# Kernel optimization log

Hardware: AMD Instinct MI355X
Metric: run time of the kernel (lower is better)

The kernel has to match this reference:

```python
import jax, jax.numpy as jnp
from jax import lax
import numpy as np


def setup_inputs() -> dict:
    key = jax.random.key(0)
    k1, k2, k3, k4, k5 = jax.random.split(key, 5)
    bs, m, v, L, P = 2, 16, 16, 40320, 32
    preds = jax.random.normal(k1, (bs, m, v, L), dtype=jnp.float32)
    target = jax.random.normal(k2, (bs, v, L), dtype=jnp.float32)
    weights = jax.random.uniform(k3, (L,), dtype=jnp.float32)
    scale = jax.random.uniform(k4, (v,), dtype=jnp.float32)
    # binary-ish patch masks over grid points (float, as in the torch buffer)
    masks = (jax.random.uniform(k5, (P, L)) < 0.25).astype(jnp.float32)
    return {"preds": preds, "target": target, "weights": weights,
            "scale": scale, "masks": masks, "beta": 1}


def _energy_score(x, y, m, beta):
    # x: (bs, m, D) ensemble, y: (bs, D) observation
    diff = x - y[:, None, :]
    a = jnp.sqrt(jnp.sum(diff * diff, axis=-1))            # (bs, m)
    score_a = jnp.mean(jnp.sum(a ** beta, axis=-1)) / m
    # pairwise distances via Gram trick (cdist p=2)
    sq = jnp.sum(x * x, axis=-1)                            # (bs, m)
    g = jnp.einsum('bid,bjd->bij', x, x)                    # (bs, m, m)
    d2 = jnp.maximum(sq[:, :, None] + sq[:, None, :] - 2.0 * g, 0.0)
    pos = d2 > 0
    d = jnp.where(pos, jnp.sqrt(jnp.where(pos, d2, 1.0)), 0.0)
    score_b = jnp.mean(jnp.sum(d ** beta, axis=(1, 2))) / (2 * m * (m - 1))
    return score_a - score_b


def reference(preds, target, weights, scale, masks, beta):
    beta = float(beta)
    bs, m, v, L = preds.shape
    # buffer scaling as in forward()
    p = preds * scale[None, None, :, None] * weights        # (bs, m, v, L)
    t = target * scale[None, :, None] * weights             # (bs, v, L)

    def body(acc, mask):
        # rearrange 'bs m v latlon -> bs m (latlon v)'
        x = (p * mask).transpose(0, 1, 3, 2).reshape(bs, m, L * v)
        y = (t * mask).transpose(0, 2, 1).reshape(bs, L * v)
        return acc + _energy_score(x, y, m, beta), None

    total, _ = lax.scan(body, jnp.float32(0.0), masks)
    return total
```

## Files before the change

### kernel.cpp

```cpp
#include <hip/hip_runtime.h>
#include <math.h>

#define BS 2
#define M 16
#define V 16
#define NROWB 136
#define NROWS 272
#define PMASK 32
#define KZ 32
#define KSTEPS 1260
#define NWORK 128

typedef __attribute__((ext_vector_type(8))) short bf16x8;
typedef __attribute__((ext_vector_type(4))) float f32x4;

static __device__ __forceinline__ unsigned short f2bf(float x) {
    unsigned int u = __float_as_uint(x);
    unsigned int r = (u + 0x7FFFu + ((u >> 16) & 1u)) >> 16;
    return (unsigned short)r;
}

template<int W>
static __device__ __forceinline__ void k1_compute(
    const float (*__restrict__ xs)[64],
    const float* __restrict__ target,
    const float* __restrict__ scale, float wl,
    int b, int lane, int l0, int L,
    unsigned short* __restrict__ S)
{
    float acc[34];
#pragma unroll
    for (int r = 0; r < 34; ++r) acc[r] = 0.0f;

    const int base = (W == 0) ? 0 : 34 * W - 16;
    const int npair = (W == 0) ? 18 : 34;
    const int aoff = (W == 0) ? 16 : 0;

    for (int v = 0; v < V; ++v) {
        float sw = scale[v] * wl;
        float x[M];
#pragma unroll
        for (int i = 0; i < M; ++i)
            x[i] = xs[i * 16 + v][lane] * sw;
        if (W == 0) {
            float y = target[(size_t)(b * V + v) * L + l0 + lane] * sw;
#pragma unroll
            for (int i = 0; i < M; ++i) {
                float d = x[i] - y;
                acc[i] = fmaf(d, d, acc[i]);
            }
        }
        int k = 0;
#pragma unroll
        for (int i = 0; i < M; ++i) {
#pragma unroll
            for (int j = i + 1; j < M; ++j) {
                if (k >= base && k < base + npair) {
                    float d = x[i] - x[j];
                    acc[aoff + k - base] = fmaf(d, d, acc[aoff + k - base]);
                }
                ++k;
            }
        }
    }
#pragma unroll
    for (int r = 0; r < 34; ++r)
        S[(size_t)(b * NROWB + 34 * W + r) * L + l0 + lane] = f2bf(acc[r]);
}

__global__ __launch_bounds__(256, 2)
void k1_pairsums(const float* __restrict__ preds, const float* __restrict__ target,
                 const float* __restrict__ weights, const float* __restrict__ scale,
                 const float* __restrict__ masks,
                 unsigned short* __restrict__ S, unsigned short* __restrict__ maskbf,
                 int L)
{
    __shared__ float xs[256][64];
    int t = (int)threadIdx.x;
    int lane = t & 63, wave = t >> 6;
    int l0 = (int)blockIdx.x * 64;
    int b = (int)blockIdx.y;

    const float* pbase = preds + (size_t)b * 256 * L + l0;
#pragma unroll
    for (int n = 0; n < 16; ++n) {
        int r0 = wave * 64 + n * 4;
        const float* g = pbase + (size_t)(r0 + (lane >> 4)) * L + (lane & 15) * 4;
        __builtin_amdgcn_global_load_lds(
            (const __attribute__((address_space(1))) unsigned int*)g,
            (__attribute__((address_space(3))) unsigned int*)&xs[r0][0],
            16, 0, 0);
    }

    if (b == 0) {
#pragma unroll
        for (int pp = 0; pp < 8; ++pp) {
            int p = wave * 8 + pp;
            maskbf[(size_t)p * L + l0 + lane] =
                (masks[(size_t)p * L + l0 + lane] != 0.0f) ? (unsigned short)0x3F80
                                                           : (unsigned short)0;
        }
    }

    float wl = weights[l0 + lane];
    __syncthreads();

    switch (wave) {
        case 0: k1_compute<0>(xs, target, scale, wl, b, lane, l0, L, S); break;
        case 1: k1_compute<1>(xs, target, scale, wl, b, lane, l0, L, S); break;
        case 2: k1_compute<2>(xs, target, scale, wl, b, lane, l0, L, S); break;
        default: k1_compute<3>(xs, target, scale, wl, b, lane, l0, L, S); break;
    }
}

__global__ __launch_bounds__(256, 4)
void k2_mfma(const unsigned short* __restrict__ S,
             const unsigned short* __restrict__ maskbf,
             float* __restrict__ D2p, int L)
{
    int lane = (int)(threadIdx.x & 63);
    int wave = (int)(threadIdx.x >> 6);
    int mtile = blockIdx.x;
    int z = blockIdx.y;
    int zw = z * 4 + wave;

    const int q = KSTEPS / NWORK;
    const int rem = KSTEPS % NWORK;
    int start = zw * q + (zw < rem ? zw : rem);
    int cnt = q + (zw < rem ? 1 : 0);

    const unsigned short* Arow =
        S + (size_t)(mtile * 16 + (lane & 15)) * L + (lane >> 4) * 8;
    const unsigned short* B0 =
        maskbf + (size_t)(lane & 15) * L + (lane >> 4) * 8;
    const unsigned short* B1 =
        maskbf + (size_t)(16 + (lane & 15)) * L + (lane >> 4) * 8;

    f32x4 acc0 = {0.f, 0.f, 0.f, 0.f};
    f32x4 acc1 = {0.f, 0.f, 0.f, 0.f};

    for (int s = 0; s < cnt; ++s) {
        int k0 = (start + s) * 32;
        bf16x8 a  = *(const bf16x8*)(Arow + k0);
        bf16x8 b0 = *(const bf16x8*)(B0 + k0);
        bf16x8 b1 = *(const bf16x8*)(B1 + k0);
        acc0 = __builtin_amdgcn_mfma_f32_16x16x32_bf16(a, b0, acc0, 0, 0, 0);
        acc1 = __builtin_amdgcn_mfma_f32_16x16x32_bf16(a, b1, acc1, 0, 0, 0);
    }

    __shared__ float red[4][512];
    int c16 = lane & 15;
#pragma unroll
    for (int reg = 0; reg < 4; ++reg) {
        int r16 = (lane >> 4) * 4 + reg;
        red[wave][r16 * 16 + c16]       = acc0[reg];
        red[wave][256 + r16 * 16 + c16] = acc1[reg];
    }
    __syncthreads();
    int t = (int)threadIdx.x;
#pragma unroll
    for (int u = t; u < 512; u += 256) {
        float v = red[0][u] + red[1][u] + red[2][u] + red[3][u];
        D2p[((size_t)z * 17 + mtile) * 512 + u] = v;
    }
}

__global__ __launch_bounds__(256, 2)
void k3_finalize(const float* __restrict__ D2p, const int* __restrict__ beta_p,
                 float* __restrict__ out)
{
    int t = (int)threadIdx.x;
    int e = blockIdx.x * 256 + t;
    int mtile = e >> 9;
    int flat = e & 511;

    float vbuf[KZ];
#pragma unroll
    for (int z = 0; z < KZ; ++z)
        vbuf[z] = D2p[((size_t)z * 17 + mtile) * 512 + flat];

    float a0 = 0.f, a1 = 0.f, a2 = 0.f, a3 = 0.f;
#pragma unroll
    for (int z = 0; z < KZ; z += 4) {
        a0 += vbuf[z + 0]; a1 += vbuf[z + 1];
        a2 += vbuf[z + 2]; a3 += vbuf[z + 3];
    }
    float d2 = fmaxf((a0 + a1) + (a2 + a3), 0.0f);
    float beta = (float)beta_p[0];
    float d = (beta == 1.0f) ? sqrtf(d2) : powf(d2, 0.5f * beta);

    const float wa = 1.0f / (float)(BS * M);
    const float wb = -1.0f / (float)(BS * M * (M - 1));
    int row = mtile * 16 + ((flat >> 4) & 15);
    int local = row % NROWB;
    float sum = ((local < M) ? wa : wb) * d;

    int lane = t & 63, wv = t >> 6;
#pragma unroll
    for (int off = 32; off > 0; off >>= 1)
        sum += __shfl_down(sum, off, 64);
    __shared__ float red[4];
    if (lane == 0) red[wv] = sum;
    __syncthreads();
    if (t == 0)
        atomicAdd(out, red[0] + red[1] + red[2] + red[3]);
}

extern "C" void kernel_launch(void* const* d_in, const int* in_sizes, int n_in,
                              void* d_out, int out_size, void* d_ws, size_t ws_size,
                              hipStream_t stream)
{
    const float* preds   = (const float*)d_in[0];
    const float* target  = (const float*)d_in[1];
    const float* weights = (const float*)d_in[2];
    const float* scale   = (const float*)d_in[3];
    const float* masks   = (const float*)d_in[4];
    const int*   beta    = (const int*)d_in[5];
    float* out = (float*)d_out;

    int L = in_sizes[2];

    unsigned short* S = (unsigned short*)d_ws;
    size_t s_bytes = (size_t)NROWS * (size_t)L * sizeof(unsigned short);
    unsigned short* maskbf = (unsigned short*)((char*)d_ws + ((s_bytes + 255) & ~(size_t)255));
    size_t m_bytes = (size_t)PMASK * (size_t)L * sizeof(unsigned short);
    float* D2p = (float*)((char*)maskbf + ((m_bytes + 255) & ~(size_t)255));

    hipMemsetAsync(out, 0, sizeof(float), stream);

    dim3 g1(L / 64, BS);
    k1_pairsums<<<g1, 256, 0, stream>>>(preds, target, weights, scale, masks,
                                        S, maskbf, L);

    dim3 g2(17, KZ);
    k2_mfma<<<g2, 256, 0, stream>>>(S, maskbf, D2p, L);

    k3_finalize<<<(NROWS * PMASK) / 256, 256, 0, stream>>>(D2p, beta, out);
}
```

Baseline: 160.8 us.

## Double-buffer preds tiles in k1 and split pair work across eight half-waves

```diff
diff --git a/kernel.cpp b/kernel.cpp
--- a/kernel.cpp
+++ b/kernel.cpp
@@ -10,6 +10,7 @@
 #define KZ 32
 #define KSTEPS 1260
 #define NWORK 128
+#define TPB 5
 
 typedef __attribute__((ext_vector_type(8))) short bf16x8;
 typedef __attribute__((ext_vector_type(4))) float f32x4;
@@ -20,30 +21,48 @@
     return (unsigned short)r;
 }
 
-template<int W>
+
+static __device__ __forceinline__ void k1_stage(
+    const float* __restrict__ preds, float* __restrict__ dst,
+    int b, int l0t, int L, int lane, int wave)
+{
+#pragma unroll
+    for (int n = 0; n < 8; ++n) {
+        int chunk = wave * 8 + n;
+        int r0 = chunk * 8;
+        const float* g = preds + (size_t)(b * 256 + r0 + (lane >> 3)) * L
+                         + l0t + (lane & 7) * 4;
+        __builtin_amdgcn_global_load_lds(
+            (const __attribute__((address_space(1))) unsigned int*)g,
+            (__attribute__((address_space(3))) unsigned int*)(dst + chunk * 256),
+            16, 0, 0);
+    }
+}
+
+template<int G>
 static __device__ __forceinline__ void k1_compute(
-    const float (*__restrict__ xs)[64],
-    const float* __restrict__ target,
+    const float* __restrict__ xsb,
+    const float* __restrict__ tg,
     const float* __restrict__ scale, float wl,
-    int b, int lane, int l0, int L,
+    int b, int li, int l, int L,
     unsigned short* __restrict__ S)
 {
-    float acc[34];
-#pragma unroll
-    for (int r = 0; r < 34; ++r) acc[r] = 0.0f;
-
-    const int base = (W == 0) ? 0 : 34 * W - 16;
-    const int npair = (W == 0) ? 18 : 34;
-    const int aoff = (W == 0) ? 16 : 0;
+    float acc[17];
+#pragma unroll
+    for (int r = 0; r < 17; ++r) acc[r] = 0.0f;
+
+    const int base = (G == 0) ? 0 : 17 * G - 16;
+    const int npair = (G == 0) ? 1 : 17;
+    const int aoff = (G == 0) ? 16 : 0;
 
     for (int v = 0; v < V; ++v) {
         float sw = scale[v] * wl;
         float x[M];
 #pragma unroll
         for (int i = 0; i < M; ++i)
-            x[i] = xs[i * 16 + v][lane] * sw;
-        if (W == 0) {
-            float y = target[(size_t)(b * V + v) * L + l0 + lane] * sw;
+            x[i] = xsb[(i * 16 + v) * 32 + li] * sw;
+        if (G == 0) {
+            float y = tg[v] * sw;
 #pragma unroll
             for (int i = 0; i < M; ++i) {
                 float d = x[i] - y;
@@ -64,8 +83,8 @@
         }
     }
 #pragma unroll
-    for (int r = 0; r < 34; ++r)
-        S[(size_t)(b * NROWB + 34 * W + r) * L + l0 + lane] = f2bf(acc[r]);
+    for (int r = 0; r < 17; ++r)
+        S[(size_t)(b * NROWB + 17 * G + r) * L + l] = f2bf(acc[r]);
 }
 
 __global__ __launch_bounds__(256, 2)
@@ -75,49 +94,70 @@
                  unsigned short* __restrict__ S, unsigned short* __restrict__ maskbf,
                  int L)
 {
-    __shared__ float xs[256][64];
+    __shared__ float xs[2][8192];
     int t = (int)threadIdx.x;
     int lane = t & 63, wave = t >> 6;
-    int l0 = (int)blockIdx.x * 64;
+    int g = t >> 5, li = t & 31;
+    int tile0 = (int)blockIdx.x * TPB;
     int b = (int)blockIdx.y;
 
-    const float* pbase = preds + (size_t)b * 256 * L + l0;
-#pragma unroll
-    for (int n = 0; n < 16; ++n) {
-        int r0 = wave * 64 + n * 4;
-        const float* g = pbase + (size_t)(r0 + (lane >> 4)) * L + (lane & 15) * 4;
-        __builtin_amdgcn_global_load_lds(
-            (const __attribute__((address_space(1))) unsigned int*)g,
-            (__attribute__((address_space(3))) unsigned int*)&xs[r0][0],
-            16, 0, 0);
-    }
-
-    if (b == 0) {
-#pragma unroll
-        for (int pp = 0; pp < 8; ++pp) {
-            int p = wave * 8 + pp;
-            maskbf[(size_t)p * L + l0 + lane] =
-                (masks[(size_t)p * L + l0 + lane] != 0.0f) ? (unsigned short)0x3F80
-                                                           : (unsigned short)0;
-        }
-    }
-
-    float wl = weights[l0 + lane];
-    __syncthreads();
-
-    switch (wave) {
-        case 0: k1_compute<0>(xs, target, scale, wl, b, lane, l0, L, S); break;
-        case 1: k1_compute<1>(xs, target, scale, wl, b, lane, l0, L, S); break;
-        case 2: k1_compute<2>(xs, target, scale, wl, b, lane, l0, L, S); break;
-        default: k1_compute<3>(xs, target, scale, wl, b, lane, l0, L, S); break;
+    k1_stage(preds, &xs[0][0], b, tile0 * 32, L, lane, wave);
+
+    for (int it = 0; it < TPB; ++it) {
+        int l0t = (tile0 + it) * 32;
+        int l = l0t + li;
+
+        float wl = weights[l];
+        float tg[V];
+        if (g == 0) {
+#pragma unroll
+            for (int v = 0; v < V; ++v)
+                tg[v] = target[(size_t)(b * V + v) * L + l];
+        }
+        unsigned short mk[4];
+        if (b == 0) {
+#pragma unroll
+            for (int pp = 0; pp < 4; ++pp) {
+                int p = g * 4 + pp;
+                mk[pp] = (masks[(size_t)p * L + l] != 0.0f) ? (unsigned short)0x3F80
+                                                            : (unsigned short)0;
+            }
+        }
+
+        __syncthreads();
+
+        if (it + 1 < TPB)
+            k1_stage(preds, &xs[(it + 1) & 1][0], b, (tile0 + it + 1) * 32, L,
+                     lane, wave);
+
+        if (b == 0) {
+#pragma unroll
+            for (int pp = 0; pp < 4; ++pp)
+                maskbf[(size_t)(g * 4 + pp) * L + l] = mk[pp];
+        }
+
+        const float* xsb = &xs[it & 1][0];
+        switch (g) {
+            case 0: k1_compute<0>(xsb, tg, scale, wl, b, li, l, L, S); break;
+            case 1: k1_compute<1>(xsb, tg, scale, wl, b, li, l, L, S); break;
+            case 2: k1_compute<2>(xsb, tg, scale, wl, b, li, l, L, S); break;
+            case 3: k1_compute<3>(xsb, tg, scale, wl, b, li, l, L, S); break;
+            case 4: k1_compute<4>(xsb, tg, scale, wl, b, li, l, L, S); break;
+            case 5: k1_compute<5>(xsb, tg, scale, wl, b, li, l, L, S); break;
+            case 6: k1_compute<6>(xsb, tg, scale, wl, b, li, l, L, S); break;
+            default: k1_compute<7>(xsb, tg, scale, wl, b, li, l, L, S); break;
+        }
     }
 }
 
 __global__ __launch_bounds__(256, 4)
 void k2_mfma(const unsigned short* __restrict__ S,
              const unsigned short* __restrict__ maskbf,
-             float* __restrict__ D2p, int L)
-{
+             float* __restrict__ D2p, float* __restrict__ out, int L)
+{
+    if (blockIdx.x == 0 && blockIdx.y == 0 && threadIdx.x == 0)
+        out[0] = 0.0f;
+
     int lane = (int)(threadIdx.x & 63);
     int wave = (int)(threadIdx.x >> 6);
     int mtile = blockIdx.x;
@@ -226,14 +266,12 @@
     size_t m_bytes = (size_t)PMASK * (size_t)L * sizeof(unsigned short);
     float* D2p = (float*)((char*)maskbf + ((m_bytes + 255) & ~(size_t)255));
 
-    hipMemsetAsync(out, 0, sizeof(float), stream);
-
-    dim3 g1(L / 64, BS);
+    dim3 g1((L / 32) / TPB, BS);
     k1_pairsums<<<g1, 256, 0, stream>>>(preds, target, weights, scale, masks,
                                         S, maskbf, L);
 
     dim3 g2(17, KZ);
-    k2_mfma<<<g2, 256, 0, stream>>>(S, maskbf, D2p, L);
+    k2_mfma<<<g2, 256, 0, stream>>>(S, maskbf, D2p, out, L);
 
     k3_finalize<<<(NROWS * PMASK) / 256, 256, 0, stream>>>(D2p, beta, out);
 }
```

New measurement: 225.7 us. +40.4%, slower.

## Stage preds in two half-variable chunks to halve LDS and raise occupancy

Applied to the files above, without the earlier changes.

```diff
diff --git a/kernel.cpp b/kernel.cpp
--- a/kernel.cpp
+++ b/kernel.cpp
@@ -20,28 +20,44 @@
     return (unsigned short)r;
 }
 
+
+static __device__ __forceinline__ void k1_stage(
+    const float* __restrict__ preds, float* __restrict__ dst,
+    int b, int v0, int l0, int L, int lane, int wave)
+{
+#pragma unroll
+    for (int n = 0; n < 8; ++n) {
+        int r0 = wave * 32 + n * 4;
+        int grow = b * 256 + (r0 >> 3) * 16 + v0 + (r0 & 7);
+        const float* g = preds + (size_t)(grow + (lane >> 4)) * L
+                         + l0 + (lane & 15) * 4;
+        __builtin_amdgcn_global_load_lds(
+            (const __attribute__((address_space(1))) unsigned int*)g,
+            (__attribute__((address_space(3))) unsigned int*)(dst + r0 * 64),
+            16, 0, 0);
+    }
+}
+
 template<int W>
-static __device__ __forceinline__ void k1_compute(
+static __device__ __forceinline__ void k1_chunk(
     const float (*__restrict__ xs)[64],
     const float* __restrict__ target,
     const float* __restrict__ scale, float wl,
-    int b, int lane, int l0, int L,
-    unsigned short* __restrict__ S)
-{
-    float acc[34];
-#pragma unroll
-    for (int r = 0; r < 34; ++r) acc[r] = 0.0f;
-
+    int b, int lane, int l0, int L, int v0,
+    float* __restrict__ acc)
+{
     const int base = (W == 0) ? 0 : 34 * W - 16;
     const int npair = (W == 0) ? 18 : 34;
     const int aoff = (W == 0) ? 16 : 0;
 
-    for (int v = 0; v < V; ++v) {
+#pragma unroll
+    for (int vc = 0; vc < 8; ++vc) {
+        int v = v0 + vc;
         float sw = scale[v] * wl;
         float x[M];
 #pragma unroll
         for (int i = 0; i < M; ++i)
-            x[i] = xs[i * 16 + v][lane] * sw;
+            x[i] = xs[i * 8 + vc][lane] * sw;
         if (W == 0) {
             float y = target[(size_t)(b * V + v) * L + l0 + lane] * sw;
 #pragma unroll
@@ -63,35 +79,24 @@
             }
         }
     }
-#pragma unroll
-    for (int r = 0; r < 34; ++r)
-        S[(size_t)(b * NROWB + 34 * W + r) * L + l0 + lane] = f2bf(acc[r]);
-}
-
-__global__ __launch_bounds__(256, 2)
+}
+
+__global__ __launch_bounds__(256, 4)
 void k1_pairsums(const float* __restrict__ preds, const float* __restrict__ target,
                  const float* __restrict__ weights, const float* __restrict__ scale,
                  const float* __restrict__ masks,
                  unsigned short* __restrict__ S, unsigned short* __restrict__ maskbf,
                  int L)
 {
-    __shared__ float xs[256][64];
+    __shared__ float xs[128][64];
     int t = (int)threadIdx.x;
     int lane = t & 63, wave = t >> 6;
     int l0 = (int)blockIdx.x * 64;
     int b = (int)blockIdx.y;
 
-    const float* pbase = preds + (size_t)b * 256 * L + l0;
-#pragma unroll
-    for (int n = 0; n < 16; ++n) {
-        int r0 = wave * 64 + n * 4;
-        const float* g = pbase + (size_t)(r0 + (lane >> 4)) * L + (lane & 15) * 4;
-        __builtin_amdgcn_global_load_lds(
-            (const __attribute__((address_space(1))) unsigned int*)g,
-            (__attribute__((address_space(3))) unsigned int*)&xs[r0][0],
-            16, 0, 0);
-    }
-
+    k1_stage(preds, &xs[0][0], b, 0, l0, L, lane, wave);
+
+    float wl = weights[l0 + lane];
     if (b == 0) {
 #pragma unroll
         for (int pp = 0; pp < 8; ++pp) {
@@ -102,22 +107,43 @@
         }
     }
 
-    float wl = weights[l0 + lane];
+    float acc[34];
+#pragma unroll
+    for (int r = 0; r < 34; ++r) acc[r] = 0.0f;
+
     __syncthreads();
 
     switch (wave) {
-        case 0: k1_compute<0>(xs, target, scale, wl, b, lane, l0, L, S); break;
-        case 1: k1_compute<1>(xs, target, scale, wl, b, lane, l0, L, S); break;
-        case 2: k1_compute<2>(xs, target, scale, wl, b, lane, l0, L, S); break;
-        default: k1_compute<3>(xs, target, scale, wl, b, lane, l0, L, S); break;
-    }
+        case 0: k1_chunk<0>(xs, target, scale, wl, b, lane, l0, L, 0, acc); break;
+        case 1: k1_chunk<1>(xs, target, scale, wl, b, lane, l0, L, 0, acc); break;
+        case 2: k1_chunk<2>(xs, target, scale, wl, b, lane, l0, L, 0, acc); break;
+        default: k1_chunk<3>(xs, target, scale, wl, b, lane, l0, L, 0, acc); break;
+    }
+
+    __syncthreads();
+    k1_stage(preds, &xs[0][0], b, 8, l0, L, lane, wave);
+    __syncthreads();
+
+    switch (wave) {
+        case 0: k1_chunk<0>(xs, target, scale, wl, b, lane, l0, L, 8, acc); break;
+        case 1: k1_chunk<1>(xs, target, scale, wl, b, lane, l0, L, 8, acc); break;
+        case 2: k1_chunk<2>(xs, target, scale, wl, b, lane, l0, L, 8, acc); break;
+        default: k1_chunk<3>(xs, target, scale, wl, b, lane, l0, L, 8, acc); break;
+    }
+
+#pragma unroll
+    for (int r = 0; r < 34; ++r)
+        S[(size_t)(b * NROWB + 34 * wave + r) * L + l0 + lane] = f2bf(acc[r]);
 }
 
 __global__ __launch_bounds__(256, 4)
 void k2_mfma(const unsigned short* __restrict__ S,
              const unsigned short* __restrict__ maskbf,
-             float* __restrict__ D2p, int L)
-{
+             float* __restrict__ D2p, float* __restrict__ out, int L)
+{
+    if (blockIdx.x == 0 && blockIdx.y == 0 && threadIdx.x == 0)
+        out[0] = 0.0f;
+
     int lane = (int)(threadIdx.x & 63);
     int wave = (int)(threadIdx.x >> 6);
     int mtile = blockIdx.x;
@@ -226,14 +252,12 @@
     size_t m_bytes = (size_t)PMASK * (size_t)L * sizeof(unsigned short);
     float* D2p = (float*)((char*)maskbf + ((m_bytes + 255) & ~(size_t)255));
 
-    hipMemsetAsync(out, 0, sizeof(float), stream);
-
     dim3 g1(L / 64, BS);
     k1_pairsums<<<g1, 256, 0, stream>>>(preds, target, weights, scale, masks,
                                         S, maskbf, L);
 
     dim3 g2(17, KZ);
-    k2_mfma<<<g2, 256, 0, stream>>>(S, maskbf, D2p, L);
+    k2_mfma<<<g2, 256, 0, stream>>>(S, maskbf, D2p, out, L);
 
     k3_finalize<<<(NROWS * PMASK) / 256, 256, 0, stream>>>(D2p, beta, out);
 }
```

Result: slower. 224.6 us (+39.7%).
